# Performance work log

Measured on AMD Instinct MI355X. Metric: run time of the kernel, lower is better.

## Reference

```python
import jax, jax.numpy as jnp
import numpy as np

B, S, D, H = 2, 2048, 1024, 16
DK = D // H
SCALE = 1.0 / np.sqrt(DK).astype(np.float32)


def setup_inputs() -> dict:
    key = jax.random.key(0)
    ks = jax.random.split(key, 7)
    std = 1.0 / np.sqrt(D).astype(np.float32)
    return {
        "query": jax.random.normal(ks[0], (B, S, D), jnp.float32),
        "key": jax.random.normal(ks[1], (B, S, D), jnp.float32),
        "value": jax.random.normal(ks[2], (B, S, D), jnp.float32),
        "Wq": jax.random.normal(ks[3], (D, D), jnp.float32) * std,
        "Wk": jax.random.normal(ks[4], (D, D), jnp.float32) * std,
        "Wv": jax.random.normal(ks[5], (D, D), jnp.float32) * std,
        "Wo": jax.random.normal(ks[6], (D, D), jnp.float32) * std,
    }


def _split_heads(x):
    # [B, S, D] -> [B, H, S, DK]
    return x.reshape(B, S, H, DK).transpose(0, 2, 1, 3)


def reference(query, key, value, Wq, Wk, Wv, Wo):
    Q = _split_heads(query @ Wq)
    K = _split_heads(key @ Wk)
    V = _split_heads(value @ Wv)
    # explicit full-score attention, as in the original (mask=None, dropout off)
    scores = jnp.einsum("bhqd,bhkd->bhqk", Q, K) * SCALE
    attn = jax.nn.softmax(scores, axis=-1)
    out = jnp.einsum("bhqk,bhkd->bhqd", attn, V)
    out = out.transpose(0, 2, 1, 3).reshape(B, S, D)  # merge heads
    return out @ Wo
```

## Files before the change

### kernel.cpp

```cpp
#include <hip/hip_runtime.h>

#define B_ 2
#define S_ 2048
#define D_ 1024
#define H_ 16

typedef unsigned short u16;
typedef unsigned long long u64;
typedef __bf16 bf16x8 __attribute__((ext_vector_type(8)));
typedef float f32x4 __attribute__((ext_vector_type(4)));
typedef unsigned short u16x8 __attribute__((ext_vector_type(8)));
typedef unsigned uint4v __attribute__((ext_vector_type(4)));

__device__ __forceinline__ unsigned swz128(unsigned o) {
  return o ^ (((o >> 7) & 7) << 4);
}

__device__ __forceinline__ void gload_lds16(const void* g, void* l) {
  __builtin_amdgcn_global_load_lds(
      (const __attribute__((address_space(1))) unsigned*)g,
      (__attribute__((address_space(3))) unsigned*)l, 16, 0, 0);
}

__device__ __forceinline__ u16 f2bf(float f) {
  union { float f; unsigned u; } v;
  v.f = f;
  unsigned u = v.u;
  return (u16)((u + 0x7fffu + ((u >> 16) & 1u)) >> 16);
}

__device__ __forceinline__ unsigned cvtpk(float lo, float hi) {
  unsigned d;
  asm("v_cvt_pk_bf16_f32 %0, %1, %2" : "=v"(d) : "v"(lo), "v"(hi));
  return d;
}

struct T4 { const float* in[4]; u16* out[4]; };
__global__ __launch_bounds__(256) void transpose_w4(T4 p) {
  __shared__ u16 t[64][65];
  const float* in = p.in[blockIdx.z];
  u16* out = p.out[blockIdx.z];
  int r0 = blockIdx.y * 64, c0 = blockIdx.x * 64;
  for (int i = threadIdx.x; i < 4096; i += 256) {
    int r = i >> 6, c = i & 63;
    t[r][c] = f2bf(in[(size_t)(r0 + r) * 1024 + c0 + c]);
  }
  __syncthreads();
  for (int i = threadIdx.x; i < 4096; i += 256) {
    int r = i >> 6, c = i & 63;
    out[(size_t)(c0 + r) * 1024 + r0 + c] = t[c][r];
  }
}

__global__ __launch_bounds__(256) void transpose_v(const u16* __restrict__ V,
                                                   u16* __restrict__ VT) {
  __shared__ u16 t[64][65];
  int s0 = blockIdx.x * 64;
  int bh = blockIdx.y, b = bh >> 4, h = bh & 15;
  const u16* src = V + (size_t)b * S_ * D_ + h * 64;
  u16* dst = VT + (size_t)bh * 64 * S_;
  for (int i = threadIdx.x; i < 4096; i += 256) {
    int s = i >> 6, dk = i & 63;
    t[s][dk] = src[(size_t)(s0 + s) * D_ + dk];
  }
  __syncthreads();
  for (int i = threadIdx.x; i < 4096; i += 256) {
    int dk = i >> 6, s = i & 63;
    dst[(size_t)dk * S_ + s0 + s] = t[s][dk];
  }
}

struct QKV { const float* A[3]; const u16* BT[3]; u16* C[3]; };
__global__ __launch_bounds__(256) void gemm_qkv(QKV p) {
  constexpr int K = 1024, N = 1024;
  __shared__ __align__(16) u16 lA[128 * 64];
  __shared__ __align__(16) u16 lB[128 * 64];
  const int tid = threadIdx.x, lane = tid & 63, w = tid >> 6;
  const int wr = w >> 1, wc = w & 1;
  const int m0 = blockIdx.x * 128, n0 = blockIdx.y * 128;
  const int g = lane >> 4, c16 = lane & 15;
  const int z = blockIdx.z;
  f32x4 acc[4][4] = {};
  const float* Af = p.A[z] + (size_t)m0 * K;
  const char* Bb = (const char*)(p.BT[z] + (size_t)n0 * K);
  u16* C = p.C[z];
  char* lAb = (char*)lA;
  char* lBb = (char*)lB;
  for (int kt = 0; kt < K; kt += 64) {
    for (int c = 0; c < 4; ++c) {
      unsigned o = c * 4096 + tid * 16;
      unsigned u = swz128(o);
      gload_lds16(Bb + (size_t)(u >> 7) * (K * 2) + kt * 2 + (u & 127), lBb + o);
    }
    for (int c = 0; c < 4; ++c) {
      unsigned o = c * 4096 + tid * 16;
      unsigned row = o >> 7, kc = (o & 127) >> 1;
      const float* s = Af + (size_t)row * K + kt + kc;
      float4 f0 = *(const float4*)s;
      float4 f1 = *(const float4*)(s + 4);
      uint4v d;
      d[0] = cvtpk(f0.x, f0.y);
      d[1] = cvtpk(f0.z, f0.w);
      d[2] = cvtpk(f1.x, f1.y);
      d[3] = cvtpk(f1.z, f1.w);
      *(uint4v*)(lAb + swz128(o)) = d;
    }
    asm volatile("s_waitcnt vmcnt(0)" ::: "memory");
    __syncthreads();
    for (int ks = 0; ks < 2; ++ks) {
      bf16x8 af[4], bf[4];
      for (int i = 0; i < 4; ++i) {
        unsigned row = wr * 64 + i * 16 + c16;
        unsigned o = row * 128 + ks * 64 + g * 16;
        af[i] = *(const bf16x8*)(lAb + (o ^ ((row & 7) << 4)));
      }
      for (int j = 0; j < 4; ++j) {
        unsigned row = wc * 64 + j * 16 + c16;
        unsigned o = row * 128 + ks * 64 + g * 16;
        bf[j] = *(const bf16x8*)(lBb + (o ^ ((row & 7) << 4)));
      }
      for (int i = 0; i < 4; ++i)
        for (int j = 0; j < 4; ++j)
          acc[i][j] = __builtin_amdgcn_mfma_f32_16x16x32_bf16(af[i], bf[j],
                                                              acc[i][j], 0, 0, 0);
    }
    __syncthreads();
  }
  for (int i = 0; i < 4; ++i)
    for (int j = 0; j < 4; ++j) {
      int row = m0 + wr * 64 + i * 16 + g * 4;
      int col = n0 + wc * 64 + j * 16 + c16;
      for (int r = 0; r < 4; ++r)
        C[(size_t)(row + r) * N + col] = f2bf(acc[i][j][r]);
    }
}

__global__ __launch_bounds__(256) void gemm_bt_f32(const u16* __restrict__ A,
                                                   const u16* __restrict__ BT,
                                                   float* __restrict__ C) {
  constexpr int K = 1024, N = 1024;
  __shared__ __align__(16) u16 lA[128 * 64];
  __shared__ __align__(16) u16 lB[64 * 64];
  const int tid = threadIdx.x, lane = tid & 63, w = tid >> 6;
  const int wr = w >> 1, wc = w & 1;
  const int m0 = blockIdx.x * 128, n0 = blockIdx.y * 64;
  const int g = lane >> 4, c16 = lane & 15;
  f32x4 acc[4][2] = {};
  const char* Ab = (const char*)(A + (size_t)m0 * K);
  const char* Bb = (const char*)(BT + (size_t)n0 * K);
  char* lAb = (char*)lA;
  char* lBb = (char*)lB;
  for (int kt = 0; kt < K; kt += 64) {
    for (int c = 0; c < 4; ++c) {
      unsigned o = w * 4096 + c * 1024 + lane * 16;
      unsigned u = swz128(o);
      gload_lds16(Ab + (size_t)(u >> 7) * (K * 2) + kt * 2 + (u & 127),
                  lAb + w * 4096 + c * 1024);
    }
    for (int c = 0; c < 2; ++c) {
      unsigned o = w * 2048 + c * 1024 + lane * 16;
      unsigned u = swz128(o);
      gload_lds16(Bb + (size_t)(u >> 7) * (K * 2) + kt * 2 + (u & 127),
                  lBb + w * 2048 + c * 1024);
    }
    asm volatile("s_waitcnt vmcnt(0)" ::: "memory");
    __syncthreads();
    for (int ks = 0; ks < 2; ++ks) {
      bf16x8 af[4], bf[2];
      for (int i = 0; i < 4; ++i) {
        unsigned row = wr * 64 + i * 16 + c16;
        unsigned o = row * 128 + ks * 64 + g * 16;
        af[i] = *(const bf16x8*)(lAb + (o ^ ((row & 7) << 4)));
      }
      for (int j = 0; j < 2; ++j) {
        unsigned row = wc * 32 + j * 16 + c16;
        unsigned o = row * 128 + ks * 64 + g * 16;
        bf[j] = *(const bf16x8*)(lBb + (o ^ ((row & 7) << 4)));
      }
      for (int i = 0; i < 4; ++i)
        for (int j = 0; j < 2; ++j)
          acc[i][j] = __builtin_amdgcn_mfma_f32_16x16x32_bf16(af[i], bf[j],
                                                              acc[i][j], 0, 0, 0);
    }
    __syncthreads();
  }
  for (int i = 0; i < 4; ++i)
    for (int j = 0; j < 2; ++j) {
      int row = m0 + wr * 64 + i * 16 + g * 4;
      int col = n0 + wc * 32 + j * 16 + c16;
      for (int r = 0; r < 4; ++r)
        C[(size_t)(row + r) * N + col] = acc[i][j][r];
    }
}

__global__ __launch_bounds__(256) void flash_attn(const u16* __restrict__ Q,
                                                  const u16* __restrict__ K,
                                                  const u16* __restrict__ VT,
                                                  u16* __restrict__ O) {
  __shared__ __align__(16) u16 lP[64 * 64];
  __shared__ __align__(16) u16 lK[2][64 * 64];
  __shared__ __align__(16) u16 lV[2][64 * 64];
  const int tid = threadIdx.x, lane = tid & 63, w = tid >> 6;
  const int g = lane >> 4, c16 = lane & 15;
  const int q0 = blockIdx.x * 64;
  const int bh = blockIdx.y, b = bh >> 4, h = bh & 15;
  const char* Qb = (const char*)(Q + (size_t)(b * S_ + q0) * D_ + h * 64);
  const char* Kb = (const char*)(K + (size_t)b * S_ * D_ + h * 64);
  const char* Vb = (const char*)(VT + (size_t)bh * 64 * S_);
  char* lPb = (char*)lP;
  char* lKb = (char*)lK;
  char* lVb = (char*)lV;

  for (int c = 0; c < 2; ++c) {
    unsigned o = w * 2048 + c * 1024 + lane * 16;
    unsigned u = swz128(o);
    gload_lds16(Qb + (size_t)(u >> 7) * (D_ * 2) + (u & 127), lPb + w * 2048 + c * 1024);
    gload_lds16(Kb + (size_t)(u >> 7) * (D_ * 2) + (u & 127), lKb + w * 2048 + c * 1024);
    gload_lds16(Vb + (size_t)(u >> 7) * (S_ * 2) + (u & 127), lVb + w * 2048 + c * 1024);
  }
  float m_run = -INFINITY, l_run = 0.f;
  f32x4 oacc[4] = {};
  asm volatile("s_waitcnt vmcnt(0)" ::: "memory");
  __syncthreads();
  bf16x8 qf[2];
  {
    unsigned row = w * 16 + c16;
    for (int ks = 0; ks < 2; ++ks) {
      unsigned o = row * 128 + ks * 64 + g * 16;
      qf[ks] = *(const bf16x8*)(lPb + swz128(o));
    }
  }
  const float SC2 = 0.125f * 1.44269504088896340736f;
  int cur = 0;
  for (int kv0 = 0; kv0 < S_; kv0 += 64, cur ^= 1) {
    char* curK = lKb + cur * 8192;
    char* curV = lVb + cur * 8192;
    if (kv0 + 64 < S_) {
      char* nK = lKb + (cur ^ 1) * 8192;
      char* nV = lVb + (cur ^ 1) * 8192;
      for (int c = 0; c < 2; ++c) {
        unsigned o = w * 2048 + c * 1024 + lane * 16;
        unsigned u = swz128(o);
        gload_lds16(Kb + (size_t)(kv0 + 64 + (u >> 7)) * (D_ * 2) + (u & 127),
                    nK + w * 2048 + c * 1024);
        gload_lds16(Vb + (size_t)(u >> 7) * (S_ * 2) + (size_t)(kv0 + 64) * 2 + (u & 127),
                    nV + w * 2048 + c * 1024);
      }
    }
    f32x4 s[4] = {};
    for (int ks = 0; ks < 2; ++ks)
      for (int j = 0; j < 4; ++j) {
        unsigned row = j * 16 + c16;
        unsigned o = row * 128 + ks * 64 + g * 16;
        bf16x8 kf = *(const bf16x8*)(curK + swz128(o));
        s[j] = __builtin_amdgcn_mfma_f32_16x16x32_bf16(kf, qf[ks], s[j], 0, 0, 0);
      }
    float rm = s[0][0];
    for (int j = 0; j < 4; ++j)
      for (int r = 0; r < 4; ++r) rm = fmaxf(rm, s[j][r]);
    rm = fmaxf(rm, __shfl_xor(rm, 16));
    rm = fmaxf(rm, __shfl_xor(rm, 32));
    if (!__all((rm - m_run) * SC2 <= 8.0f)) {
      float mn = fmaxf(m_run, rm);
      float sc = exp2f((m_run - mn) * SC2);
      l_run *= sc;
      for (int i = 0; i < 4; ++i) oacc[i] *= sc;
      m_run = mn;
    }
    float rs = 0.f;
    unsigned qrow = w * 16 + c16;
    for (int j = 0; j < 4; ++j) {
      float p0 = exp2f((s[j][0] - m_run) * SC2);
      float p1 = exp2f((s[j][1] - m_run) * SC2);
      float p2 = exp2f((s[j][2] - m_run) * SC2);
      float p3 = exp2f((s[j][3] - m_run) * SC2);
      rs += (p0 + p1) + (p2 + p3);
      unsigned w0 = cvtpk(p0, p1);
      unsigned w1 = cvtpk(p2, p3);
      unsigned o = qrow * 128 + (unsigned)(j * 16 + g * 4) * 2;
      *(u64*)(lPb + swz128(o)) = (u64)w0 | ((u64)w1 << 32);
    }
    rs += __shfl_xor(rs, 16);
    rs += __shfl_xor(rs, 32);
    l_run += rs;
    for (int ks = 0; ks < 2; ++ks) {
      unsigned po = qrow * 128 + ks * 64 + g * 16;
      bf16x8 pf = *(const bf16x8*)(lPb + swz128(po));
      for (int i = 0; i < 4; ++i) {
        unsigned vo = (unsigned)(i * 16 + c16) * 128 + ks * 64 + g * 16;
        bf16x8 vf = *(const bf16x8*)(curV + swz128(vo));
        oacc[i] = __builtin_amdgcn_mfma_f32_16x16x32_bf16(vf, pf, oacc[i], 0, 0, 0);
      }
    }
    asm volatile("s_waitcnt vmcnt(0)" ::: "memory");
    __syncthreads();
  }
  float inv = 1.f / l_run;
  int q = q0 + w * 16 + c16;
  u16* orow = O + (size_t)(b * S_ + q) * D_ + h * 64;
  for (int i = 0; i < 4; ++i) {
    unsigned e0 = cvtpk(oacc[i][0] * inv, oacc[i][1] * inv);
    unsigned e1 = cvtpk(oacc[i][2] * inv, oacc[i][3] * inv);
    *(u64*)(orow + i * 16 + g * 4) = (u64)e0 | ((u64)e1 << 32);
  }
}

extern "C" void kernel_launch(void* const* d_in, const int* in_sizes, int n_in,
                              void* d_out, int out_size, void* d_ws, size_t ws_size,
                              hipStream_t stream) {
  const float* q_in = (const float*)d_in[0];
  const float* k_in = (const float*)d_in[1];
  const float* v_in = (const float*)d_in[2];
  const float* Wq = (const float*)d_in[3];
  const float* Wk = (const float*)d_in[4];
  const float* Wv = (const float*)d_in[5];
  const float* Wo = (const float*)d_in[6];
  u16* ws = (u16*)d_ws;
  const size_t WSZ = (size_t)1024 * 1024;
  const size_t TSZ = (size_t)B_ * S_ * D_;
  u16* WqT = ws;
  u16* WkT = ws + WSZ;
  u16* WvT = ws + 2 * WSZ;
  u16* WoT = ws + 3 * WSZ;
  u16* Qb = ws + 4 * WSZ;
  u16* Kb = Qb + TSZ;
  u16* Vb = Kb + TSZ;
  u16* VTb = Vb + TSZ;
  u16* Ob = VTb + TSZ;
  dim3 tb(256);
  T4 tw = {{Wq, Wk, Wv, Wo}, {WqT, WkT, WvT, WoT}};
  transpose_w4<<<dim3(16, 16, 4), tb, 0, stream>>>(tw);
  QKV gq = {{q_in, k_in, v_in}, {WqT, WkT, WvT}, {Qb, Kb, Vb}};
  gemm_qkv<<<dim3(32, 8, 3), tb, 0, stream>>>(gq);
  transpose_v<<<dim3(32, 32), tb, 0, stream>>>(Vb, VTb);
  flash_attn<<<dim3(S_ / 64, B_ * H_), tb, 0, stream>>>(Qb, Kb, VTb, Ob);
  gemm_bt_f32<<<dim3(32, 16), tb, 0, stream>>>(Ob, WoT, (float*)d_out);
}
```

Baseline: 168.1 us.

## Fuse V transpose into QKV GEMM epilogue, add XCD block swizzle and MFMA priority

The V projection now writes its output directly in the transposed per-head layout from the GEMM epilogue, which removes the separate transpose_v kernel launch and one round trip of V through memory. Block indices in the QKV GEMM, output GEMM and attention kernels are remapped so that neighbouring tiles land on the same XCD, aiming for better L2 reuse. The attention kernel also raises wave priority around its MFMA sections. The fused epilogue stores 4-element vectors along the sequence axis, which may be less coalesced than the row-major stores it replaces.

```diff
diff --git a/kernel.cpp b/kernel.cpp
--- a/kernel.cpp
+++ b/kernel.cpp
@@ -10,10 +10,15 @@
 typedef __bf16 bf16x8 __attribute__((ext_vector_type(8)));
 typedef float f32x4 __attribute__((ext_vector_type(4)));
 typedef unsigned short u16x8 __attribute__((ext_vector_type(8)));
+typedef unsigned short u16x4 __attribute__((ext_vector_type(4)));
 typedef unsigned uint4v __attribute__((ext_vector_type(4)));
 
 __device__ __forceinline__ unsigned swz128(unsigned o) {
   return o ^ (((o >> 7) & 7) << 4);
+}
+
+__device__ __forceinline__ unsigned xcd_swz(unsigned id, unsigned cpx) {
+  return (id & 7) * cpx + (id >> 3);
 }
 
 __device__ __forceinline__ void gload_lds16(const void* g, void* l) {
@@ -52,38 +57,21 @@
   }
 }
 
-__global__ __launch_bounds__(256) void transpose_v(const u16* __restrict__ V,
-                                                   u16* __restrict__ VT) {
-  __shared__ u16 t[64][65];
-  int s0 = blockIdx.x * 64;
-  int bh = blockIdx.y, b = bh >> 4, h = bh & 15;
-  const u16* src = V + (size_t)b * S_ * D_ + h * 64;
-  u16* dst = VT + (size_t)bh * 64 * S_;
-  for (int i = threadIdx.x; i < 4096; i += 256) {
-    int s = i >> 6, dk = i & 63;
-    t[s][dk] = src[(size_t)(s0 + s) * D_ + dk];
-  }
-  __syncthreads();
-  for (int i = threadIdx.x; i < 4096; i += 256) {
-    int dk = i >> 6, s = i & 63;
-    dst[(size_t)dk * S_ + s0 + s] = t[s][dk];
-  }
-}
-
-struct QKV { const float* A[3]; const u16* BT[3]; u16* C[3]; };
+struct QKV { const float* A[3]; const u16* BT[3]; u16* C[2]; u16* VT; };
 __global__ __launch_bounds__(256) void gemm_qkv(QKV p) {
   constexpr int K = 1024, N = 1024;
   __shared__ __align__(16) u16 lA[128 * 64];
   __shared__ __align__(16) u16 lB[128 * 64];
   const int tid = threadIdx.x, lane = tid & 63, w = tid >> 6;
   const int wr = w >> 1, wc = w & 1;
-  const int m0 = blockIdx.x * 128, n0 = blockIdx.y * 128;
+  unsigned id = blockIdx.x + blockIdx.y * 32 + blockIdx.z * 256;
+  unsigned sw = xcd_swz(id, 96);
+  const int z = sw >> 8;
+  const int m0 = (sw & 31) * 128, n0 = ((sw >> 5) & 7) * 128;
   const int g = lane >> 4, c16 = lane & 15;
-  const int z = blockIdx.z;
   f32x4 acc[4][4] = {};
   const float* Af = p.A[z] + (size_t)m0 * K;
   const char* Bb = (const char*)(p.BT[z] + (size_t)n0 * K);
-  u16* C = p.C[z];
   char* lAb = (char*)lA;
   char* lBb = (char*)lB;
   for (int kt = 0; kt < K; kt += 64) {
@@ -126,13 +114,30 @@
     }
     __syncthreads();
   }
-  for (int i = 0; i < 4; ++i)
-    for (int j = 0; j < 4; ++j) {
-      int row = m0 + wr * 64 + i * 16 + g * 4;
-      int col = n0 + wc * 64 + j * 16 + c16;
-      for (int r = 0; r < 4; ++r)
-        C[(size_t)(row + r) * N + col] = f2bf(acc[i][j][r]);
-    }
+  if (z < 2) {
+    u16* C = p.C[z];
+    for (int i = 0; i < 4; ++i)
+      for (int j = 0; j < 4; ++j) {
+        int row = m0 + wr * 64 + i * 16 + g * 4;
+        int col = n0 + wc * 64 + j * 16 + c16;
+        for (int r = 0; r < 4; ++r)
+          C[(size_t)(row + r) * N + col] = f2bf(acc[i][j][r]);
+      }
+  } else {
+    for (int i = 0; i < 4; ++i)
+      for (int j = 0; j < 4; ++j) {
+        int row = m0 + wr * 64 + i * 16 + g * 4;
+        int col = n0 + wc * 64 + j * 16 + c16;
+        int b = row >> 11, s0 = row & 2047;
+        int bh = b * 16 + (col >> 6), dk = col & 63;
+        u16x4 ov;
+        ov[0] = f2bf(acc[i][j][0]);
+        ov[1] = f2bf(acc[i][j][1]);
+        ov[2] = f2bf(acc[i][j][2]);
+        ov[3] = f2bf(acc[i][j][3]);
+        *(u16x4*)(p.VT + ((size_t)bh * 64 + dk) * S_ + s0) = ov;
+      }
+  }
 }
 
 __global__ __launch_bounds__(256) void gemm_bt_f32(const u16* __restrict__ A,
@@ -143,7 +148,9 @@
   __shared__ __align__(16) u16 lB[64 * 64];
   const int tid = threadIdx.x, lane = tid & 63, w = tid >> 6;
   const int wr = w >> 1, wc = w & 1;
-  const int m0 = blockIdx.x * 128, n0 = blockIdx.y * 64;
+  unsigned id = blockIdx.x + blockIdx.y * 32;
+  unsigned sw = xcd_swz(id, 64);
+  const int m0 = (sw & 31) * 128, n0 = (sw >> 5) * 64;
   const int g = lane >> 4, c16 = lane & 15;
   f32x4 acc[4][2] = {};
   const char* Ab = (const char*)(A + (size_t)m0 * K);
@@ -202,8 +209,10 @@
   __shared__ __align__(16) u16 lV[2][64 * 64];
   const int tid = threadIdx.x, lane = tid & 63, w = tid >> 6;
   const int g = lane >> 4, c16 = lane & 15;
-  const int q0 = blockIdx.x * 64;
-  const int bh = blockIdx.y, b = bh >> 4, h = bh & 15;
+  unsigned id = blockIdx.x + blockIdx.y * gridDim.x;
+  unsigned sw = xcd_swz(id, 128);
+  const int q0 = (sw & 31) * 64;
+  const int bh = sw >> 5, b = bh >> 4, h = bh & 15;
   const char* Qb = (const char*)(Q + (size_t)(b * S_ + q0) * D_ + h * 64);
   const char* Kb = (const char*)(K + (size_t)b * S_ * D_ + h * 64);
   const char* Vb = (const char*)(VT + (size_t)bh * 64 * S_);
@@ -248,6 +257,7 @@
       }
     }
     f32x4 s[4] = {};
+    __builtin_amdgcn_s_setprio(1);
     for (int ks = 0; ks < 2; ++ks)
       for (int j = 0; j < 4; ++j) {
         unsigned row = j * 16 + c16;
@@ -255,6 +265,7 @@
         bf16x8 kf = *(const bf16x8*)(curK + swz128(o));
         s[j] = __builtin_amdgcn_mfma_f32_16x16x32_bf16(kf, qf[ks], s[j], 0, 0, 0);
       }
+    __builtin_amdgcn_s_setprio(0);
     float rm = s[0][0];
     for (int j = 0; j < 4; ++j)
       for (int r = 0; r < 4; ++r) rm = fmaxf(rm, s[j][r]);
@@ -283,6 +294,7 @@
     rs += __shfl_xor(rs, 16);
     rs += __shfl_xor(rs, 32);
     l_run += rs;
+    __builtin_amdgcn_s_setprio(1);
     for (int ks = 0; ks < 2; ++ks) {
       unsigned po = qrow * 128 + ks * 64 + g * 16;
       bf16x8 pf = *(const bf16x8*)(lPb + swz128(po));
@@ -292,6 +304,7 @@
         oacc[i] = __builtin_amdgcn_mfma_f32_16x16x32_bf16(vf, pf, oacc[i], 0, 0, 0);
       }
     }
+    __builtin_amdgcn_s_setprio(0);
     asm volatile("s_waitcnt vmcnt(0)" ::: "memory");
     __syncthreads();
   }
@@ -324,15 +337,13 @@
   u16* WoT = ws + 3 * WSZ;
   u16* Qb = ws + 4 * WSZ;
   u16* Kb = Qb + TSZ;
-  u16* Vb = Kb + TSZ;
-  u16* VTb = Vb + TSZ;
+  u16* VTb = Kb + TSZ;
   u16* Ob = VTb + TSZ;
   dim3 tb(256);
   T4 tw = {{Wq, Wk, Wv, Wo}, {WqT, WkT, WvT, WoT}};
   transpose_w4<<<dim3(16, 16, 4), tb, 0, stream>>>(tw);
-  QKV gq = {{q_in, k_in, v_in}, {WqT, WkT, WvT}, {Qb, Kb, Vb}};
+  QKV gq = {{q_in, k_in, v_in}, {WqT, WkT, WvT}, {Qb, Kb}, VTb};
   gemm_qkv<<<dim3(32, 8, 3), tb, 0, stream>>>(gq);
-  transpose_v<<<dim3(32, 32), tb, 0, stream>>>(Vb, VTb);
-  flash_attn<<<dim3(S_ / 64, B_ * H_), tb, 0, stream>>>(Qb, Kb, VTb, Ob);
+  flash_attn<<<dim3(32, 32), tb, 0, stream>>>(Qb, Kb, VTb, Ob);
   gemm_bt_f32<<<dim3(32, 16), tb, 0, stream>>>(Ob, WoT, (float*)d_out);
 }
```

After: 173.5 us. 3.2% more time.
